# Optimization experiments

Measured on AMD Instinct MI355X. Metric: run time of the kernel, lower is better.

## Reference

```python
import jax, jax.numpy as jnp
import numpy as np

N = 10000
K = 16
MEAN_NODES = 625.0  # N / K


def setup_inputs() -> dict:
    key = jax.random.key(0)
    k1, k2, k3 = jax.random.split(key, 3)
    # Y: soft partition assignments [N, K]; keep strictly positive so gamma > 0
    Y = jax.random.uniform(k1, (N, K), dtype=jnp.float32, minval=0.01, maxval=1.0)
    # A: dense adjacency / edge-weight matrix [N, N]
    A = jax.random.uniform(k2, (N, N), dtype=jnp.float32)
    # degree: per-node degree column vector [N, 1]
    degree = jax.random.uniform(k3, (N, 1), dtype=jnp.float32, minval=0.5, maxval=2.0)
    return {"Y": Y, "A": A, "degree": degree}


def reference(Y, A, degree):
    # gamma_k = sum_i Y[i,k] * degree[i]  -> [K, 1]
    gamma = Y.T @ degree                      # [K, 1]
    Yn = Y / gamma.reshape(1, K)              # divide column k by gamma_k, [N, K]
    # error_cut = sum_ij A_ij * (Yn @ (1 - Y^T))_ij
    error_cut = ((Yn @ (1.0 - Y.T)) * A).sum()
    # error_partition = sum_k (sum_i Y[i,k] - mean_nodes)^2
    col_sums = Y.sum(axis=0)                  # [K]
    error_partition = jnp.square(col_sums - MEAN_NODES).sum()
    return error_cut + error_partition
```

## Files before the change

### kernel.cpp

```cpp
#include <hip/hip_runtime.h>

#define N_NODES 10000
#define K_COLS 16
#define MEAN_NODES 625.0f

#define WS_YT_OFF 32

__global__ __launch_bounds__(256) void prep_reduce(const float* __restrict__ Y,
                                                   const float* __restrict__ deg,
                                                   float* __restrict__ ws,
                                                   float* __restrict__ out) {
    const int t = threadIdx.x;
    float g[K_COLS], c[K_COLS];
#pragma unroll
    for (int k = 0; k < K_COLS; ++k) { g[k] = 0.f; c[k] = 0.f; }

    for (int i = t; i < N_NODES; i += 256) {
        float d = deg[i];
        const float4* yp = (const float4*)(Y + (size_t)i * K_COLS);
        float y[K_COLS];
        *(float4*)(y + 0)  = yp[0];
        *(float4*)(y + 4)  = yp[1];
        *(float4*)(y + 8)  = yp[2];
        *(float4*)(y + 12) = yp[3];
#pragma unroll
        for (int k = 0; k < K_COLS; ++k) { g[k] += y[k] * d; c[k] += y[k]; }
    }

#pragma unroll
    for (int k = 0; k < K_COLS; ++k) {
        for (int off = 32; off > 0; off >>= 1) {
            g[k] += __shfl_down(g[k], off);
            c[k] += __shfl_down(c[k], off);
        }
    }

    __shared__ float red[4][32];
    const int wave = t >> 6, lane = t & 63;
    if (lane == 0) {
#pragma unroll
        for (int k = 0; k < K_COLS; ++k) {
            red[wave][k] = g[k];
            red[wave][K_COLS + k] = c[k];
        }
    }
    __syncthreads();

    if (t < 32) {
        float v = red[0][t] + red[1][t] + red[2][t] + red[3][t];
        if (t < 16) {
            ws[t] = 1.0f / v;
        } else {
            float dlt = v - MEAN_NODES;
            float sq = dlt * dlt;
            for (int off = 8; off > 0; off >>= 1) sq += __shfl_down(sq, off, 16);
            if (t == 16) out[0] = sq;
        }
    }
}

__global__ __launch_bounds__(256) void prep_transpose(const float* __restrict__ Y,
                                                      float* __restrict__ yt) {
    const int i = blockIdx.x * 256 + threadIdx.x;
    if (i < N_NODES) {
        const float4* yp = (const float4*)(Y + (size_t)i * K_COLS);
        float y[K_COLS];
        *(float4*)(y + 0)  = yp[0];
        *(float4*)(y + 4)  = yp[1];
        *(float4*)(y + 8)  = yp[2];
        *(float4*)(y + 12) = yp[3];
#pragma unroll
        for (int k = 0; k < K_COLS; ++k) yt[(size_t)k * N_NODES + i] = y[k];
    }
}

#define STEPS_PER_SEG 8

__global__ __launch_bounds__(256) void gap_main(const float* __restrict__ A,
                                                const float* __restrict__ Y,
                                                const float* __restrict__ ws,
                                                float* __restrict__ out) {
    const float* __restrict__ YT = ws + WS_YT_OFF;
    const int wave = threadIdx.x >> 6;
    const int lane = threadIdx.x & 63;
    const int rowbase = blockIdx.x * 16 + wave * 4;

    float acc[4][K_COLS];
    float rowsum[4];
#pragma unroll
    for (int r = 0; r < 4; ++r) {
        rowsum[r] = 0.f;
#pragma unroll
        for (int k = 0; k < K_COLS; ++k) acc[r][k] = 0.f;
    }

    const int stepbase = blockIdx.y * STEPS_PER_SEG;
    const size_t arow_off = (size_t)rowbase * N_NODES;

#pragma unroll 1
    for (int s = 0; s < STEPS_PER_SEG; ++s) {
        const int j0 = ((stepbase + s) << 8) + (lane << 2);
        if (j0 < N_NODES) {
            const float* arow = A + arow_off + j0;
            const float4 a0 = *(const float4*)(arow);
            const float4 a1 = *(const float4*)(arow + N_NODES);
            const float4 a2 = *(const float4*)(arow + 2 * (size_t)N_NODES);
            const float4 a3 = *(const float4*)(arow + 3 * (size_t)N_NODES);

            rowsum[0] += (a0.x + a0.y) + (a0.z + a0.w);
            rowsum[1] += (a1.x + a1.y) + (a1.z + a1.w);
            rowsum[2] += (a2.x + a2.y) + (a2.z + a2.w);
            rowsum[3] += (a3.x + a3.y) + (a3.z + a3.w);

            const float* ytp = YT + j0;
#pragma unroll
            for (int k = 0; k < K_COLS; ++k) {
                const float4 y = *(const float4*)(ytp + (size_t)k * N_NODES);
                acc[0][k] += a0.x * y.x + a0.y * y.y + a0.z * y.z + a0.w * y.w;
                acc[1][k] += a1.x * y.x + a1.y * y.y + a1.z * y.z + a1.w * y.w;
                acc[2][k] += a2.x * y.x + a2.y * y.y + a2.z * y.z + a2.w * y.w;
                acc[3][k] += a3.x * y.x + a3.y * y.y + a3.z * y.z + a3.w * y.w;
            }
        }
    }

    __shared__ float rgs[K_COLS];
    if (threadIdx.x < K_COLS) rgs[threadIdx.x] = ws[threadIdx.x];
    __syncthreads();

    float partial = 0.f;
#pragma unroll
    for (int r = 0; r < 4; ++r) {
        const int row = rowbase + r;
        const float* yrow = Y + (size_t)row * K_COLS;
        float s_i = 0.f, dotv = 0.f;
#pragma unroll
        for (int k = 0; k < K_COLS; ++k) {
            const float yn = yrow[k] * rgs[k];
            s_i += yn;
            dotv += yn * acc[r][k];
        }
        partial += s_i * rowsum[r] - dotv;
    }

    for (int off = 32; off > 0; off >>= 1) partial += __shfl_down(partial, off);
    __shared__ float wpart[4];
    if (lane == 0) wpart[wave] = partial;
    __syncthreads();
    if (threadIdx.x == 0)
        atomicAdd(out, (wpart[0] + wpart[1]) + (wpart[2] + wpart[3]));
}

extern "C" void kernel_launch(void* const* d_in, const int* in_sizes, int n_in,
                              void* d_out, int out_size, void* d_ws, size_t ws_size,
                              hipStream_t stream) {
    const float* Y   = (const float*)d_in[0];
    const float* A   = (const float*)d_in[1];
    const float* deg = (const float*)d_in[2];
    float* out = (float*)d_out;
    float* ws  = (float*)d_ws;

    hipLaunchKernelGGL(prep_reduce, dim3(1), dim3(256), 0, stream, Y, deg, ws, out);
    hipLaunchKernelGGL(prep_transpose, dim3((N_NODES + 255) / 256), dim3(256), 0, stream,
                       Y, ws + WS_YT_OFF);
    hipLaunchKernelGGL(gap_main, dim3(N_NODES / 16, 5), dim3(256), 0, stream,
                       A, Y, ws, out);
}
```

Before: 609.1 us.

## Parallelize prep reduction across blocks and software-prefetch A tiles in main loop

Replaces the single-block gamma/column-sum reduction and the separate transpose kernel with a 40-block kernel that does the transpose and writes per-block partial sums, followed by a tiny finalize kernel. The main kernel now double-buffers the A float4 loads, issuing the next step's loads before computing the current step, so memory latency overlaps with FMAs. The single-block serial reduction was a latency bottleneck. Prefetching adds register pressure and performs dummy loads at index 0 for invalid steps.

```diff
diff --git a/kernel.cpp b/kernel.cpp
--- a/kernel.cpp
+++ b/kernel.cpp
@@ -4,28 +4,38 @@
 #define K_COLS 16
 #define MEAN_NODES 625.0f
 
-#define WS_YT_OFF 32
+#define WS_PART_OFF 64
+#define WS_YT_OFF 4096
+#define PREP_BLOCKS 40
 
-__global__ __launch_bounds__(256) void prep_reduce(const float* __restrict__ Y,
-                                                   const float* __restrict__ deg,
-                                                   float* __restrict__ ws,
-                                                   float* __restrict__ out) {
+__global__ __launch_bounds__(256) void prep_partial(const float* __restrict__ Y,
+                                                    const float* __restrict__ deg,
+                                                    float* __restrict__ ws) {
+    const int b = blockIdx.x;
     const int t = threadIdx.x;
-    float g[K_COLS], c[K_COLS];
-#pragma unroll
-    for (int k = 0; k < K_COLS; ++k) { g[k] = 0.f; c[k] = 0.f; }
+    const int i = b * 250 + t;
+    const bool valid = (t < 250);
 
-    for (int i = t; i < N_NODES; i += 256) {
-        float d = deg[i];
+    float y[K_COLS];
+    float d = 0.f;
+    if (valid) {
+        d = deg[i];
         const float4* yp = (const float4*)(Y + (size_t)i * K_COLS);
-        float y[K_COLS];
         *(float4*)(y + 0)  = yp[0];
         *(float4*)(y + 4)  = yp[1];
         *(float4*)(y + 8)  = yp[2];
         *(float4*)(y + 12) = yp[3];
+        float* yt = ws + WS_YT_OFF;
 #pragma unroll
-        for (int k = 0; k < K_COLS; ++k) { g[k] += y[k] * d; c[k] += y[k]; }
+        for (int k = 0; k < K_COLS; ++k) yt[(size_t)k * N_NODES + i] = y[k];
+    } else {
+#pragma unroll
+        for (int k = 0; k < K_COLS; ++k) y[k] = 0.f;
     }
+
+    float g[K_COLS], c[K_COLS];
+#pragma unroll
+    for (int k = 0; k < K_COLS; ++k) { g[k] = y[k] * d; c[k] = y[k]; }
 
 #pragma unroll
     for (int k = 0; k < K_COLS; ++k) {
@@ -48,6 +58,17 @@
 
     if (t < 32) {
         float v = red[0][t] + red[1][t] + red[2][t] + red[3][t];
+        ws[WS_PART_OFF + b * 32 + t] = v;
+    }
+}
+
+__global__ __launch_bounds__(64) void prep_final(float* __restrict__ ws,
+                                                 float* __restrict__ out) {
+    const int t = threadIdx.x;
+    if (t < 32) {
+        float v = 0.f;
+#pragma unroll
+        for (int b = 0; b < PREP_BLOCKS; ++b) v += ws[WS_PART_OFF + b * 32 + t];
         if (t < 16) {
             ws[t] = 1.0f / v;
         } else {
@@ -56,21 +77,6 @@
             for (int off = 8; off > 0; off >>= 1) sq += __shfl_down(sq, off, 16);
             if (t == 16) out[0] = sq;
         }
-    }
-}
-
-__global__ __launch_bounds__(256) void prep_transpose(const float* __restrict__ Y,
-                                                      float* __restrict__ yt) {
-    const int i = blockIdx.x * 256 + threadIdx.x;
-    if (i < N_NODES) {
-        const float4* yp = (const float4*)(Y + (size_t)i * K_COLS);
-        float y[K_COLS];
-        *(float4*)(y + 0)  = yp[0];
-        *(float4*)(y + 4)  = yp[1];
-        *(float4*)(y + 8)  = yp[2];
-        *(float4*)(y + 12) = yp[3];
-#pragma unroll
-        for (int k = 0; k < K_COLS; ++k) yt[(size_t)k * N_NODES + i] = y[k];
     }
 }
 
@@ -94,34 +100,54 @@
         for (int k = 0; k < K_COLS; ++k) acc[r][k] = 0.f;
     }
 
-    const int stepbase = blockIdx.y * STEPS_PER_SEG;
-    const size_t arow_off = (size_t)rowbase * N_NODES;
+    const float* __restrict__ Abase = A + (size_t)rowbase * N_NODES;
+    const int jstart = (blockIdx.y * STEPS_PER_SEG << 8) + (lane << 2);
+
+    bool v_cur = jstart < N_NODES;
+    int jc_cur = v_cur ? jstart : 0;
+    float4 a0, a1, a2, a3;
+    {
+        const float* p = Abase + jc_cur;
+        a0 = *(const float4*)(p);
+        a1 = *(const float4*)(p + N_NODES);
+        a2 = *(const float4*)(p + 2 * (size_t)N_NODES);
+        a3 = *(const float4*)(p + 3 * (size_t)N_NODES);
+        if (!v_cur) {
+            a0 = a1 = a2 = a3 = make_float4(0.f, 0.f, 0.f, 0.f);
+        }
+    }
 
 #pragma unroll 1
     for (int s = 0; s < STEPS_PER_SEG; ++s) {
-        const int j0 = ((stepbase + s) << 8) + (lane << 2);
-        if (j0 < N_NODES) {
-            const float* arow = A + arow_off + j0;
-            const float4 a0 = *(const float4*)(arow);
-            const float4 a1 = *(const float4*)(arow + N_NODES);
-            const float4 a2 = *(const float4*)(arow + 2 * (size_t)N_NODES);
-            const float4 a3 = *(const float4*)(arow + 3 * (size_t)N_NODES);
+        const int jnext = jstart + ((s + 1) << 8);
+        const bool v_next = (s + 1 < STEPS_PER_SEG) && (jnext < N_NODES);
+        const int jc_next = v_next ? jnext : 0;
+        const float* pn = Abase + jc_next;
+        float4 b0 = *(const float4*)(pn);
+        float4 b1 = *(const float4*)(pn + N_NODES);
+        float4 b2 = *(const float4*)(pn + 2 * (size_t)N_NODES);
+        float4 b3 = *(const float4*)(pn + 3 * (size_t)N_NODES);
+        if (!v_next) {
+            b0 = b1 = b2 = b3 = make_float4(0.f, 0.f, 0.f, 0.f);
+        }
 
-            rowsum[0] += (a0.x + a0.y) + (a0.z + a0.w);
-            rowsum[1] += (a1.x + a1.y) + (a1.z + a1.w);
-            rowsum[2] += (a2.x + a2.y) + (a2.z + a2.w);
-            rowsum[3] += (a3.x + a3.y) + (a3.z + a3.w);
+        rowsum[0] += (a0.x + a0.y) + (a0.z + a0.w);
+        rowsum[1] += (a1.x + a1.y) + (a1.z + a1.w);
+        rowsum[2] += (a2.x + a2.y) + (a2.z + a2.w);
+        rowsum[3] += (a3.x + a3.y) + (a3.z + a3.w);
 
-            const float* ytp = YT + j0;
+        const float* ytp = YT + jc_cur;
 #pragma unroll
-            for (int k = 0; k < K_COLS; ++k) {
-                const float4 y = *(const float4*)(ytp + (size_t)k * N_NODES);
-                acc[0][k] += a0.x * y.x + a0.y * y.y + a0.z * y.z + a0.w * y.w;
-                acc[1][k] += a1.x * y.x + a1.y * y.y + a1.z * y.z + a1.w * y.w;
-                acc[2][k] += a2.x * y.x + a2.y * y.y + a2.z * y.z + a2.w * y.w;
-                acc[3][k] += a3.x * y.x + a3.y * y.y + a3.z * y.z + a3.w * y.w;
-            }
+        for (int k = 0; k < K_COLS; ++k) {
+            const float4 y = *(const float4*)(ytp + (size_t)k * N_NODES);
+            acc[0][k] += a0.x * y.x + a0.y * y.y + a0.z * y.z + a0.w * y.w;
+            acc[1][k] += a1.x * y.x + a1.y * y.y + a1.z * y.z + a1.w * y.w;
+            acc[2][k] += a2.x * y.x + a2.y * y.y + a2.z * y.z + a2.w * y.w;
+            acc[3][k] += a3.x * y.x + a3.y * y.y + a3.z * y.z + a3.w * y.w;
         }
+
+        a0 = b0; a1 = b1; a2 = b2; a3 = b3;
+        jc_cur = jc_next;
     }
 
     __shared__ float rgs[K_COLS];
@@ -160,9 +186,8 @@
     float* out = (float*)d_out;
     float* ws  = (float*)d_ws;
 
-    hipLaunchKernelGGL(prep_reduce, dim3(1), dim3(256), 0, stream, Y, deg, ws, out);
-    hipLaunchKernelGGL(prep_transpose, dim3((N_NODES + 255) / 256), dim3(256), 0, stream,
-                       Y, ws + WS_YT_OFF);
+    hipLaunchKernelGGL(prep_partial, dim3(PREP_BLOCKS), dim3(256), 0, stream, Y, deg, ws);
+    hipLaunchKernelGGL(prep_final, dim3(1), dim3(64), 0, stream, ws, out);
     hipLaunchKernelGGL(gap_main, dim3(N_NODES / 16, 5), dim3(256), 0, stream,
                        A, Y, ws, out);
 }
```

After: 564.4 us. 7.3% less time.
